# Performance work log

Hardware: AMD Instinct MI355X
Metric: run time of the kernel (lower is better)

Reference implementation:

```python
import jax, jax.numpy as jnp
import numpy as np

B, C, H, W = 4, 512, 64, 64          # visual feature map
NTXT, TDIM, HEADS = 256, 1024, 8     # context tokens, textual dim, heads
DHEAD = TDIM // HEADS


def setup_inputs() -> dict:
    key = jax.random.key(0)
    ks = jax.random.split(key, 8)
    x = jax.random.normal(ks[0], (B, C, H, W), dtype=jnp.float32)
    timesteps = jax.random.randint(ks[1], (B,), 0, 1000)
    context = jax.random.normal(ks[2], (B, NTXT, TDIM), dtype=jnp.float32)
    # Linear weights stored as (in, out) so y = x @ W (matches torch x @ W.T)
    s = 0.02
    Wq = jax.random.normal(ks[3], (TDIM, TDIM), dtype=jnp.float32) * s
    Wk = jax.random.normal(ks[4], (C, TDIM), dtype=jnp.float32) * s
    Wv = jax.random.normal(ks[5], (C, TDIM), dtype=jnp.float32) * s
    Wo = jax.random.normal(ks[6], (TDIM, TDIM), dtype=jnp.float32) * s
    bo = jnp.zeros((TDIM,), dtype=jnp.float32)
    return {"x": x, "timesteps": timesteps, "context": context,
            "Wq": Wq, "Wk": Wk, "Wv": Wv, "Wo": Wo, "bo": bo}


def reference(x, timesteps, context, Wq, Wk, Wv, Wo, bo):
    b, c, h, w = x.shape
    # b c h w -> b (h w) c
    vis = x.reshape(b, c, h * w).transpose(0, 2, 1)
    q = context @ Wq                       # [b, ntxt, tdim]
    k = vis @ Wk                           # [b, hw, tdim]
    v = vis @ Wv                           # [b, hw, tdim]
    def split_heads(t):
        bb, n, _ = t.shape
        return t.reshape(bb, n, HEADS, DHEAD).transpose(0, 2, 1, 3)  # b h n d
    q, k, v = map(split_heads, (q, k, v))
    scale = DHEAD ** -0.5
    sim = jnp.einsum('bhid,bhjd->bhij', q, k) * scale   # [b,h,ntxt,hw]
    attn = jax.nn.softmax(sim, axis=-1)
    out = jnp.einsum('bhij,bhjd->bhid', attn, v)        # [b,h,ntxt,d]
    out = out.transpose(0, 2, 1, 3).reshape(b, -1, TDIM)  # b n (h d)
    return out @ Wo + bo                                  # dropout p=0 is identity
```

## Files before the change

### kernel.cpp

```cpp
#include <hip/hip_runtime.h>

typedef __attribute__((ext_vector_type(8))) short short8;
typedef __attribute__((ext_vector_type(4))) float f32x4;
typedef __attribute__((ext_vector_type(4))) int int4v;

#define DEV static __device__ __forceinline__

DEV float bf2f(unsigned short u) { return __uint_as_float(((unsigned)u) << 16); }
DEV unsigned short f2bf(float f) {
  unsigned u = __float_as_uint(f);
  u = (u + 0x7FFFu + ((u >> 16) & 1u)) >> 16;
  return (unsigned short)u;
}

__global__ __launch_bounds__(256) void k_cast_bf16(const float* __restrict__ in,
                                                   unsigned short* __restrict__ out) {
  long i = ((long)blockIdx.x * 256 + threadIdx.x) * 4;
  float4 v = *(const float4*)(in + i);
  ushort4 o;
  o.x = f2bf(v.x); o.y = f2bf(v.y); o.z = f2bf(v.z); o.w = f2bf(v.w);
  *(ushort4*)(out + i) = o;
}

__global__ __launch_bounds__(256) void k_transpose_cast(const float* __restrict__ in,
                                                        unsigned short* __restrict__ out,
                                                        int R, int Cc, long sInZ, long sOutZ) {
  __shared__ float t[32][33];
  long zi = (long)blockIdx.z * sInZ, zo = (long)blockIdx.z * sOutZ;
  int c0 = blockIdx.x * 32, r0 = blockIdx.y * 32;
  int tx = threadIdx.x & 31, ty = threadIdx.x >> 5;
#pragma unroll
  for (int i = 0; i < 4; ++i)
    t[ty + 8 * i][tx] = in[zi + (long)(r0 + ty + 8 * i) * Cc + c0 + tx];
  __syncthreads();
#pragma unroll
  for (int i = 0; i < 4; ++i)
    out[zo + (long)(c0 + ty + 8 * i) * R + r0 + tx] = f2bf(t[tx][ty + 8 * i]);
}

__global__ __launch_bounds__(256) void k_gemm(
    const unsigned short* __restrict__ A, const unsigned short* __restrict__ B,
    void* __restrict__ Cout, const float* __restrict__ bias,
    int K, int lda, int ldb, int ldc,
    long sAb, long sAh, long sBb, long sBh, long sCb, long sCh, int epi) {
  __shared__ __align__(16) char lds[32768];
  char* As = lds;
  char* Bs = lds + 16384;
  int z = blockIdx.z, zb = z >> 3, zh = z & 7;
  const unsigned short* Ab = A + (long)zb * sAb + (long)zh * sAh;
  const unsigned short* Bb = B + (long)zb * sBb + (long)zh * sBh;
  int tid = threadIdx.x;
  int m0 = blockIdx.x * 128, n0 = blockIdx.y * 128;
  int lane = tid & 63, wid = tid >> 6;
  int wm = (wid >> 1) * 64, wn = (wid & 1) * 64;
  int l15 = lane & 15, lg = lane >> 4;
  int srow = tid >> 3, sg = tid & 7;

  f32x4 acc[4][4];
#pragma unroll
  for (int i = 0; i < 4; ++i)
#pragma unroll
    for (int j = 0; j < 4; ++j)
      acc[i][j] = (f32x4){0.f, 0.f, 0.f, 0.f};

  for (int k0 = 0; k0 < K; k0 += 64) {
    __syncthreads();
#pragma unroll
    for (int p = 0; p < 4; ++p) {
      int r = srow + 32 * p;
      int4v va = *(const int4v*)(Ab + (long)(m0 + r) * lda + k0 + sg * 8);
      *(int4v*)(As + r * 128 + ((sg * 16) ^ ((r & 7) << 4))) = va;
      int4v vb = *(const int4v*)(Bb + (long)(n0 + r) * ldb + k0 + sg * 8);
      *(int4v*)(Bs + r * 128 + ((sg * 16) ^ ((r & 7) << 4))) = vb;
    }
    __syncthreads();
#pragma unroll
    for (int ks = 0; ks < 2; ++ks) {
      short8 af[4], bfr[4];
#pragma unroll
      for (int t = 0; t < 4; ++t) {
        int mr = wm + t * 16 + l15;
        af[t] = *(const short8*)(As + mr * 128 + (((lg * 16) + ks * 64) ^ ((mr & 7) << 4)));
        int nr = wn + t * 16 + l15;
        bfr[t] = *(const short8*)(Bs + nr * 128 + (((lg * 16) + ks * 64) ^ ((nr & 7) << 4)));
      }
#pragma unroll
      for (int mt = 0; mt < 4; ++mt)
#pragma unroll
        for (int nt = 0; nt < 4; ++nt)
          acc[mt][nt] = __builtin_amdgcn_mfma_f32_16x16x32_bf16(af[mt], bfr[nt], acc[mt][nt], 0, 0, 0);
    }
  }

  long cbase = (long)zb * sCb + (long)zh * sCh;
#pragma unroll
  for (int mt = 0; mt < 4; ++mt) {
#pragma unroll
    for (int r = 0; r < 4; ++r) {
      long row = m0 + wm + mt * 16 + lg * 4 + r;
      long rowoff = cbase + row * (long)ldc;
#pragma unroll
      for (int nt = 0; nt < 4; ++nt) {
        int col = n0 + wn + nt * 16 + l15;
        float v = acc[mt][nt][r];
        if (epi == 0)
          ((unsigned short*)Cout)[rowoff + col] = f2bf(v);
        else
          ((float*)Cout)[rowoff + col] = v + bias[col];
      }
    }
  }
}

__global__ __launch_bounds__(256) void k_transpose_v(const unsigned short* __restrict__ KV,
                                                     unsigned short* __restrict__ Vt) {
  __shared__ __align__(16) char tl[64 * 144];
  int b = blockIdx.z;
  int t0 = blockIdx.x * 64;
  int h0 = blockIdx.y * 64;
  int g = threadIdx.x & 7, r = threadIdx.x >> 3;
  const unsigned short* src = KV + (long)b * 4096 * 2048 + 1024;
#pragma unroll
  for (int p = 0; p < 2; ++p) {
    int hw = r + 32 * p;
    short8 vv = *(const short8*)(src + (long)(h0 + hw) * 2048 + t0 + g * 8);
    *(short8*)(tl + hw * 144 + ((g * 16) ^ (((hw >> 3) & 7) << 4))) = vv;
  }
  __syncthreads();
  unsigned short* dst = Vt + (long)b * 1024 * 4096;
#pragma unroll
  for (int p = 0; p < 2; ++p) {
    int tr = r + 32 * p;
    short8 ov;
#pragma unroll
    for (int j = 0; j < 8; ++j) {
      int hw = g * 8 + j;
      ov[j] = *(const short*)(tl + hw * 144 + ((tr * 2) ^ (((hw >> 3) & 7) << 4)));
    }
    *(short8*)(dst + (long)(t0 + tr) * 4096 + h0 + g * 8) = ov;
  }
}

__global__ __launch_bounds__(512) void k_flash(
    const unsigned short* __restrict__ Qb, const unsigned short* __restrict__ KV,
    const unsigned short* __restrict__ Vt, float* __restrict__ Po,
    float* __restrict__ Pm, float* __restrict__ Pl) {
  __shared__ __align__(16) char lds[49152];
  char* Ks = lds;
  char* Vs = lds + 16384;
  char* Ps = lds + 32768;
  int qt = blockIdx.x, sp = blockIdx.y, bh = blockIdx.z;
  int b = bh >> 3, h = bh & 7;
  int tid = threadIdx.x, lane = tid & 63, wid = tid >> 6;
  int l15 = lane & 15, lg = lane >> 4;
  const float cs = 0.08838834764831845f * 1.4426950408889634f;

  int qrow = qt * 128 + wid * 16 + l15;
  const unsigned short* qp = Qb + ((long)(b * 256 + qrow)) * 1024 + h * 128;
  short8 qf[4];
#pragma unroll
  for (int dt = 0; dt < 4; ++dt)
    qf[dt] = *(const short8*)(qp + dt * 32 + lg * 8);

  f32x4 acc_o[8];
#pragma unroll
  for (int i = 0; i < 8; ++i) acc_o[i] = (f32x4){0.f, 0.f, 0.f, 0.f};
  float m_r[4], l_r[4];
#pragma unroll
  for (int r = 0; r < 4; ++r) { m_r[r] = -1e30f; l_r[r] = 0.f; }

  const unsigned short* kvb = KV + (long)b * 4096 * 2048 + h * 128;
  const unsigned short* vtb = Vt + (long)b * 1024 * 4096 + (long)h * 128 * 4096;
  char* pw = Ps + wid * 2048;
  int kc = tid & 15, kr = tid >> 4;
  int vc = tid & 7, vr = tid >> 3;

  for (int it = 0; it < 16; ++it) {
    int kv0 = sp * 1024 + it * 64;
    __syncthreads();
#pragma unroll
    for (int p = 0; p < 2; ++p) {
      int r = kr + 32 * p;
      int4v v = *(const int4v*)(kvb + (long)(kv0 + r) * 2048 + kc * 8);
      *(int4v*)(Ks + r * 256 + ((kc * 16) ^ ((r & 7) << 4))) = v;
      int d = vr + 64 * p;
      int4v v2 = *(const int4v*)(vtb + (long)d * 4096 + kv0 + vc * 8);
      *(int4v*)(Vs + d * 128 + ((vc * 16) ^ ((d & 7) << 4))) = v2;
    }
    __syncthreads();

    f32x4 s[4];
#pragma unroll
    for (int t = 0; t < 4; ++t) s[t] = (f32x4){0.f, 0.f, 0.f, 0.f};
#pragma unroll
    for (int t = 0; t < 4; ++t) {
      int krow = t * 16 + l15;
#pragma unroll
      for (int dt = 0; dt < 4; ++dt) {
        short8 kf = *(const short8*)(Ks + krow * 256 + ((dt * 64 + lg * 16) ^ ((krow & 7) << 4)));
        s[t] = __builtin_amdgcn_mfma_f32_16x16x32_bf16(qf[dt], kf, s[t], 0, 0, 0);
      }
    }

    float pm[4];
#pragma unroll
    for (int r = 0; r < 4; ++r)
      pm[r] = fmaxf(fmaxf(s[0][r], s[1][r]), fmaxf(s[2][r], s[3][r])) * cs;
#pragma unroll
    for (int o = 1; o < 16; o <<= 1)
#pragma unroll
      for (int r = 0; r < 4; ++r) pm[r] = fmaxf(pm[r], __shfl_xor(pm[r], o));
    float cf[4], rs[4];
#pragma unroll
    for (int r = 0; r < 4; ++r) {
      float mn = fmaxf(m_r[r], pm[r]);
      cf[r] = exp2f(m_r[r] - mn);
      m_r[r] = mn;
      rs[r] = 0.f;
    }
#pragma unroll
    for (int t = 0; t < 4; ++t) {
#pragma unroll
      for (int r = 0; r < 4; ++r) {
        float p = exp2f(s[t][r] * cs - m_r[r]);
        rs[r] += p;
        int q = lg * 4 + r;
        *(unsigned short*)(pw + q * 128 + ((t * 32 + l15 * 2) ^ ((q & 7) << 4))) = f2bf(p);
      }
    }
#pragma unroll
    for (int o = 1; o < 16; o <<= 1)
#pragma unroll
      for (int r = 0; r < 4; ++r) rs[r] += __shfl_xor(rs[r], o);
#pragma unroll
    for (int r = 0; r < 4; ++r) l_r[r] = l_r[r] * cf[r] + rs[r];
#pragma unroll
    for (int dt = 0; dt < 8; ++dt)
#pragma unroll
      for (int r = 0; r < 4; ++r) acc_o[dt][r] *= cf[r];

    short8 pa0 = *(const short8*)(pw + l15 * 128 + ((lg * 16) ^ ((l15 & 7) << 4)));
    short8 pa1 = *(const short8*)(pw + l15 * 128 + ((64 + lg * 16) ^ ((l15 & 7) << 4)));
#pragma unroll
    for (int dt = 0; dt < 8; ++dt) {
      int vrow = dt * 16 + l15;
      short8 vb0 = *(const short8*)(Vs + vrow * 128 + ((lg * 16) ^ ((vrow & 7) << 4)));
      short8 vb1 = *(const short8*)(Vs + vrow * 128 + ((64 + lg * 16) ^ ((vrow & 7) << 4)));
      acc_o[dt] = __builtin_amdgcn_mfma_f32_16x16x32_bf16(pa0, vb0, acc_o[dt], 0, 0, 0);
      acc_o[dt] = __builtin_amdgcn_mfma_f32_16x16x32_bf16(pa1, vb1, acc_o[dt], 0, 0, 0);
    }
  }

  int qbase = qt * 128 + wid * 16;
  long pobase = (long)((sp * 32 + bh) * 256) * 128;
#pragma unroll
  for (int dt = 0; dt < 8; ++dt)
#pragma unroll
    for (int r = 0; r < 4; ++r) {
      int q = qbase + lg * 4 + r;
      Po[pobase + (long)q * 128 + dt * 16 + l15] = acc_o[dt][r];
    }
  if (l15 == 0) {
#pragma unroll
    for (int r = 0; r < 4; ++r) {
      int q = qbase + lg * 4 + r;
      Pm[(sp * 32 + bh) * 256 + q] = m_r[r];
      Pl[(sp * 32 + bh) * 256 + q] = l_r[r];
    }
  }
}

__global__ __launch_bounds__(256) void k_combine(const float* __restrict__ Po,
                                                 const float* __restrict__ Pm,
                                                 const float* __restrict__ Pl,
                                                 unsigned short* __restrict__ AOut) {
  int gid = blockIdx.x * 256 + threadIdx.x;
  int row = gid >> 5, dg = gid & 31;
  int bh = row >> 8, q = row & 255;
  int b = bh >> 3, h = bh & 7;
  int mi = bh * 256 + q;
  const int ms = 32 * 256;
  float m0 = Pm[mi], m1 = Pm[ms + mi], m2 = Pm[2 * ms + mi], m3 = Pm[3 * ms + mi];
  float mx = fmaxf(fmaxf(m0, m1), fmaxf(m2, m3));
  float w0 = exp2f(m0 - mx), w1 = exp2f(m1 - mx), w2 = exp2f(m2 - mx), w3 = exp2f(m3 - mx);
  float denom = Pl[mi] * w0 + Pl[ms + mi] * w1 + Pl[2 * ms + mi] * w2 + Pl[3 * ms + mi] * w3;
  float inv = 1.f / denom;
  long base = (long)row * 128 + dg * 4;
  long stride = (long)32 * 256 * 128;
  f32x4 o0 = *(const f32x4*)(Po + base);
  f32x4 o1 = *(const f32x4*)(Po + base + stride);
  f32x4 o2 = *(const f32x4*)(Po + base + 2 * stride);
  f32x4 o3 = *(const f32x4*)(Po + base + 3 * stride);
  ushort4 res;
#pragma unroll
  for (int i = 0; i < 4; ++i) {
    float v = (o0[i] * w0 + o1[i] * w1 + o2[i] * w2 + o3[i] * w3) * inv;
    ((unsigned short*)&res)[i] = f2bf(v);
  }
  *(ushort4*)(AOut + ((long)(b * 256 + q)) * 1024 + h * 128 + dg * 4) = res;
}

extern "C" void kernel_launch(void* const* d_in, const int* in_sizes, int n_in,
                              void* d_out, int out_size, void* d_ws, size_t ws_size,
                              hipStream_t stream) {
  const float* x   = (const float*)d_in[0];
  const float* ctx = (const float*)d_in[2];
  const float* Wq  = (const float*)d_in[3];
  const float* Wk  = (const float*)d_in[4];
  const float* Wv  = (const float*)d_in[5];
  const float* Wo  = (const float*)d_in[6];
  const float* bo  = (const float*)d_in[7];
  float* out = (float*)d_out;

  char* w = (char*)d_ws;
  auto alloc = [&](long bytes) { char* p = w; w += (bytes + 255) & ~255L; return p; };
  unsigned short* xT   = (unsigned short*)alloc((long)4 * 4096 * 512 * 2);
  unsigned short* WqT  = (unsigned short*)alloc((long)1024 * 1024 * 2);
  unsigned short* WkvT = (unsigned short*)alloc((long)2048 * 512 * 2);
  unsigned short* WoT  = (unsigned short*)alloc((long)1024 * 1024 * 2);
  unsigned short* ctxb = (unsigned short*)alloc((long)4 * 256 * 1024 * 2);
  unsigned short* Qb   = (unsigned short*)alloc((long)4 * 256 * 1024 * 2);
  unsigned short* KV   = (unsigned short*)alloc((long)4 * 4096 * 2048 * 2);
  unsigned short* Vt   = (unsigned short*)alloc((long)4 * 1024 * 4096 * 2);
  float*          Po   = (float*)alloc((long)4 * 32 * 256 * 128 * 4);
  float*          Pm   = (float*)alloc((long)4 * 32 * 256 * 4);
  float*          Pl   = (float*)alloc((long)4 * 32 * 256 * 4);
  unsigned short* AOut = (unsigned short*)alloc((long)4 * 256 * 1024 * 2);

  k_cast_bf16<<<1024, 256, 0, stream>>>(ctx, ctxb);
  k_transpose_cast<<<dim3(32, 32, 1), 256, 0, stream>>>(Wq, WqT, 1024, 1024, 0, 0);
  k_transpose_cast<<<dim3(32, 16, 1), 256, 0, stream>>>(Wk, WkvT, 512, 1024, 0, 0);
  k_transpose_cast<<<dim3(32, 16, 1), 256, 0, stream>>>(Wv, WkvT + 1024 * 512, 512, 1024, 0, 0);
  k_transpose_cast<<<dim3(32, 32, 1), 256, 0, stream>>>(Wo, WoT, 1024, 1024, 0, 0);
  k_transpose_cast<<<dim3(128, 16, 4), 256, 0, stream>>>(x, xT, 512, 4096,
                                                         (long)512 * 4096, (long)4096 * 512);

  k_gemm<<<dim3(8, 8, 1), 256, 0, stream>>>(ctxb, WqT, Qb, nullptr,
      1024, 1024, 1024, 1024, 0, 0, 0, 0, 0, 0, 0);
  k_gemm<<<dim3(128, 16, 1), 256, 0, stream>>>(xT, WkvT, KV, nullptr,
      512, 512, 512, 2048, 0, 0, 0, 0, 0, 0, 0);
  k_transpose_v<<<dim3(16, 64, 4), 256, 0, stream>>>(KV, Vt);
  k_flash<<<dim3(2, 4, 32), 512, 0, stream>>>(Qb, KV, Vt, Po, Pm, Pl);
  k_combine<<<1024, 256, 0, stream>>>(Po, Pm, Pl, AOut);
  k_gemm<<<dim3(8, 8, 1), 256, 0, stream>>>(AOut, WoT, out, bo,
      1024, 1024, 1024, 1024, 0, 0, 0, 0, 0, 0, 1);
}
```

Before: 284.1 us.

## Use direct global-to-LDS loads, double-buffer flash tiles, and double KV splits

Replaces register-staged global loads with global_load_lds DMA in both the GEMM and the flash kernel, pre-swizzling source columns so the LDS layout stays conflict-free. The flash kernel now double-buffers its K/V tiles so the next tile's loads overlap the current tile's compute, with one barrier per iteration. The KV dimension is split 8 ways instead of 4, giving 512 blocks, and the combine kernel and partial buffers grow to match. The aim is to hide memory latency and raise occupancy, at the cost of 80KB LDS per flash block and a heavier combine pass.

```diff
diff --git a/kernel.cpp b/kernel.cpp
--- a/kernel.cpp
+++ b/kernel.cpp
@@ -11,6 +11,12 @@
   unsigned u = __float_as_uint(f);
   u = (u + 0x7FFFu + ((u >> 16) & 1u)) >> 16;
   return (unsigned short)u;
+}
+
+DEV void gload_lds16(const void* g, void* l) {
+  __builtin_amdgcn_global_load_lds(
+      (const __attribute__((address_space(1))) void*)g,
+      (__attribute__((address_space(3))) void*)l, 16, 0, 0);
 }
 
 __global__ __launch_bounds__(256) void k_cast_bf16(const float* __restrict__ in,
@@ -54,7 +60,6 @@
   int lane = tid & 63, wid = tid >> 6;
   int wm = (wid >> 1) * 64, wn = (wid & 1) * 64;
   int l15 = lane & 15, lg = lane >> 4;
-  int srow = tid >> 3, sg = tid & 7;
 
   f32x4 acc[4][4];
 #pragma unroll
@@ -67,11 +72,10 @@
     __syncthreads();
 #pragma unroll
     for (int p = 0; p < 4; ++p) {
-      int r = srow + 32 * p;
-      int4v va = *(const int4v*)(Ab + (long)(m0 + r) * lda + k0 + sg * 8);
-      *(int4v*)(As + r * 128 + ((sg * 16) ^ ((r & 7) << 4))) = va;
-      int4v vb = *(const int4v*)(Bb + (long)(n0 + r) * ldb + k0 + sg * 8);
-      *(int4v*)(Bs + r * 128 + ((sg * 16) ^ ((r & 7) << 4))) = vb;
+      int r = (wid * 4 + p) * 8 + (lane >> 3);
+      int cs8 = ((lane & 7) ^ (r & 7)) * 8;
+      gload_lds16(Ab + (long)(m0 + r) * lda + k0 + cs8, As + (wid * 4 + p) * 1024);
+      gload_lds16(Bb + (long)(n0 + r) * ldb + k0 + cs8, Bs + (wid * 4 + p) * 1024);
     }
     __syncthreads();
 #pragma unroll
@@ -145,16 +149,19 @@
     const unsigned short* __restrict__ Qb, const unsigned short* __restrict__ KV,
     const unsigned short* __restrict__ Vt, float* __restrict__ Po,
     float* __restrict__ Pm, float* __restrict__ Pl) {
-  __shared__ __align__(16) char lds[49152];
+  __shared__ __align__(16) char lds[81920];
   char* Ks = lds;
-  char* Vs = lds + 16384;
-  char* Ps = lds + 32768;
+  char* Vs = lds + 32768;
+  char* Ps = lds + 65536;
   int qt = blockIdx.x, sp = blockIdx.y, bh = blockIdx.z;
   int b = bh >> 3, h = bh & 7;
   int tid = threadIdx.x, lane = tid & 63, wid = tid >> 6;
   int l15 = lane & 15, lg = lane >> 4;
   const float cs = 0.08838834764831845f * 1.4426950408889634f;
 
+  const unsigned short* kvb = KV + (long)b * 4096 * 2048 + h * 128;
+  const unsigned short* vtb = Vt + (long)b * 1024 * 4096 + (long)h * 128 * 4096;
+
   int qrow = qt * 128 + wid * 16 + l15;
   const unsigned short* qp = Qb + ((long)(b * 256 + qrow)) * 1024 + h * 128;
   short8 qf[4];
@@ -169,25 +176,32 @@
 #pragma unroll
   for (int r = 0; r < 4; ++r) { m_r[r] = -1e30f; l_r[r] = 0.f; }
 
-  const unsigned short* kvb = KV + (long)b * 4096 * 2048 + h * 128;
-  const unsigned short* vtb = Vt + (long)b * 1024 * 4096 + (long)h * 128 * 4096;
   char* pw = Ps + wid * 2048;
-  int kc = tid & 15, kr = tid >> 4;
-  int vc = tid & 7, vr = tid >> 3;
-
-  for (int it = 0; it < 16; ++it) {
-    int kv0 = sp * 1024 + it * 64;
-    __syncthreads();
+  int krK = lane >> 4, kcK = lane & 15;
+  int krV = lane >> 3, kcV = lane & 7;
+
+  auto stage = [&](int it, int buf) {
+    int kv0 = sp * 512 + it * 64;
+    char* kb = Ks + (buf << 14);
+    char* vb = Vs + (buf << 14);
 #pragma unroll
     for (int p = 0; p < 2; ++p) {
-      int r = kr + 32 * p;
-      int4v v = *(const int4v*)(kvb + (long)(kv0 + r) * 2048 + kc * 8);
-      *(int4v*)(Ks + r * 256 + ((kc * 16) ^ ((r & 7) << 4))) = v;
-      int d = vr + 64 * p;
-      int4v v2 = *(const int4v*)(vtb + (long)d * 4096 + kv0 + vc * 8);
-      *(int4v*)(Vs + d * 128 + ((vc * 16) ^ ((d & 7) << 4))) = v2;
-    }
-    __syncthreads();
+      int seg = wid * 2 + p;
+      int r = seg * 4 + krK;
+      gload_lds16(kvb + (long)(kv0 + r) * 2048 + ((kcK ^ (r & 7)) * 8), kb + seg * 1024);
+      int d = seg * 8 + krV;
+      gload_lds16(vtb + (long)d * 4096 + kv0 + ((kcV ^ (d & 7)) * 8), vb + seg * 1024);
+    }
+  };
+
+  stage(0, 0);
+  __syncthreads();
+  int cur = 0;
+
+  for (int it = 0; it < 8; ++it) {
+    if (it + 1 < 8) stage(it + 1, cur ^ 1);
+    const char* Kc = Ks + (cur << 14);
+    const char* Vc = Vs + (cur << 14);
 
     f32x4 s[4];
 #pragma unroll
@@ -197,7 +211,7 @@
       int krow = t * 16 + l15;
 #pragma unroll
       for (int dt = 0; dt < 4; ++dt) {
-        short8 kf = *(const short8*)(Ks + krow * 256 + ((dt * 64 + lg * 16) ^ ((krow & 7) << 4)));
+        short8 kf = *(const short8*)(Kc + krow * 256 + ((dt * 64 + lg * 16) ^ ((krow & 7) << 4)));
         s[t] = __builtin_amdgcn_mfma_f32_16x16x32_bf16(qf[dt], kf, s[t], 0, 0, 0);
       }
     }
@@ -244,11 +258,13 @@
 #pragma unroll
     for (int dt = 0; dt < 8; ++dt) {
       int vrow = dt * 16 + l15;
-      short8 vb0 = *(const short8*)(Vs + vrow * 128 + ((lg * 16) ^ ((vrow & 7) << 4)));
-      short8 vb1 = *(const short8*)(Vs + vrow * 128 + ((64 + lg * 16) ^ ((vrow & 7) << 4)));
+      short8 vb0 = *(const short8*)(Vc + vrow * 128 + ((lg * 16) ^ ((vrow & 7) << 4)));
+      short8 vb1 = *(const short8*)(Vc + vrow * 128 + ((64 + lg * 16) ^ ((vrow & 7) << 4)));
       acc_o[dt] = __builtin_amdgcn_mfma_f32_16x16x32_bf16(pa0, vb0, acc_o[dt], 0, 0, 0);
       acc_o[dt] = __builtin_amdgcn_mfma_f32_16x16x32_bf16(pa1, vb1, acc_o[dt], 0, 0, 0);
     }
+    __syncthreads();
+    cur ^= 1;
   }
 
   int qbase = qt * 128 + wid * 16;
@@ -280,23 +296,30 @@
   int b = bh >> 3, h = bh & 7;
   int mi = bh * 256 + q;
   const int ms = 32 * 256;
-  float m0 = Pm[mi], m1 = Pm[ms + mi], m2 = Pm[2 * ms + mi], m3 = Pm[3 * ms + mi];
-  float mx = fmaxf(fmaxf(m0, m1), fmaxf(m2, m3));
-  float w0 = exp2f(m0 - mx), w1 = exp2f(m1 - mx), w2 = exp2f(m2 - mx), w3 = exp2f(m3 - mx);
-  float denom = Pl[mi] * w0 + Pl[ms + mi] * w1 + Pl[2 * ms + mi] * w2 + Pl[3 * ms + mi] * w3;
+  float m[8];
+  float mx = -1e30f;
+#pragma unroll
+  for (int s = 0; s < 8; ++s) { m[s] = Pm[s * ms + mi]; mx = fmaxf(mx, m[s]); }
+  float wgt[8];
+  float denom = 0.f;
+#pragma unroll
+  for (int s = 0; s < 8; ++s) {
+    wgt[s] = exp2f(m[s] - mx);
+    denom += Pl[s * ms + mi] * wgt[s];
+  }
   float inv = 1.f / denom;
   long base = (long)row * 128 + dg * 4;
-  long stride = (long)32 * 256 * 128;
-  f32x4 o0 = *(const f32x4*)(Po + base);
-  f32x4 o1 = *(const f32x4*)(Po + base + stride);
-  f32x4 o2 = *(const f32x4*)(Po + base + 2 * stride);
-  f32x4 o3 = *(const f32x4*)(Po + base + 3 * stride);
+  const long stride = (long)32 * 256 * 128;
+  f32x4 acc = (f32x4){0.f, 0.f, 0.f, 0.f};
+#pragma unroll
+  for (int s = 0; s < 8; ++s) {
+    f32x4 o = *(const f32x4*)(Po + base + s * stride);
+#pragma unroll
+    for (int i = 0; i < 4; ++i) acc[i] += o[i] * wgt[s];
+  }
   ushort4 res;
 #pragma unroll
-  for (int i = 0; i < 4; ++i) {
-    float v = (o0[i] * w0 + o1[i] * w1 + o2[i] * w2 + o3[i] * w3) * inv;
-    ((unsigned short*)&res)[i] = f2bf(v);
-  }
+  for (int i = 0; i < 4; ++i) ((unsigned short*)&res)[i] = f2bf(acc[i] * inv);
   *(ushort4*)(AOut + ((long)(b * 256 + q)) * 1024 + h * 128 + dg * 4) = res;
 }
 
@@ -322,9 +345,9 @@
   unsigned short* Qb   = (unsigned short*)alloc((long)4 * 256 * 1024 * 2);
   unsigned short* KV   = (unsigned short*)alloc((long)4 * 4096 * 2048 * 2);
   unsigned short* Vt   = (unsigned short*)alloc((long)4 * 1024 * 4096 * 2);
-  float*          Po   = (float*)alloc((long)4 * 32 * 256 * 128 * 4);
-  float*          Pm   = (float*)alloc((long)4 * 32 * 256 * 4);
-  float*          Pl   = (float*)alloc((long)4 * 32 * 256 * 4);
+  float*          Po   = (float*)alloc((long)8 * 32 * 256 * 128 * 4);
+  float*          Pm   = (float*)alloc((long)8 * 32 * 256 * 4);
+  float*          Pl   = (float*)alloc((long)8 * 32 * 256 * 4);
   unsigned short* AOut = (unsigned short*)alloc((long)4 * 256 * 1024 * 2);
 
   k_cast_bf16<<<1024, 256, 0, stream>>>(ctx, ctxb);
@@ -340,7 +363,7 @@
   k_gemm<<<dim3(128, 16, 1), 256, 0, stream>>>(xT, WkvT, KV, nullptr,
       512, 512, 512, 2048, 0, 0, 0, 0, 0, 0, 0);
   k_transpose_v<<<dim3(16, 64, 4), 256, 0, stream>>>(KV, Vt);
-  k_flash<<<dim3(2, 4, 32), 512, 0, stream>>>(Qb, KV, Vt, Po, Pm, Pl);
+  k_flash<<<dim3(2, 8, 32), 512, 0, stream>>>(Qb, KV, Vt, Po, Pm, Pl);
   k_combine<<<1024, 256, 0, stream>>>(Po, Pm, Pl, AOut);
   k_gemm<<<dim3(8, 8, 1), 256, 0, stream>>>(AOut, WoT, out, bo,
       1024, 1024, 1024, 1024, 0, 0, 0, 0, 0, 0, 1);
```

Result: faster. 272.0 us (-4.3%).
